# Kernel optimization log

Hardware: AMD Instinct MI355X
Metric: run time of the kernel (lower is better)

Reference implementation:

```python
import jax, jax.numpy as jnp
import numpy as np

B, N, NC, DIM, H, D, M, TOPK = 1, 2048, 2048, 1024, 16, 64, 16, 64


def _l2norm(t):
    # F.normalize(t, p=2, dim=-1)
    return t / jnp.clip(jnp.linalg.norm(t, axis=-1, keepdims=True), 1e-12)


def _attn_layer(x, ctx, q_mask, k_mask, Wq, Wk, Wv, th_pre, th_post,
                mem_k, mem_v, scale_p, hs, Wo):
    b, n, _ = x.shape
    h, m, d = mem_k.shape
    nc = ctx.shape[1]
    q = (x @ Wq).reshape(b, n, h, d).transpose(0, 2, 1, 3)      # b h i d
    k = (ctx @ Wk).reshape(b, nc, h, d).transpose(0, 2, 1, 3)   # b h j d
    v = (ctx @ Wv).reshape(b, nc, h, d).transpose(0, 2, 1, 3)
    # memory key/values prepended
    k = jnp.concatenate([jnp.broadcast_to(mem_k[None], (b, h, m, d)), k], axis=2)
    v = jnp.concatenate([jnp.broadcast_to(mem_v[None], (b, h, m, d)), v], axis=2)
    # input mask (q_mask x k_mask), padded True over mem slots
    im = q_mask[:, None, :, None] & k_mask[:, None, None, :]    # b 1 i j
    im = jnp.pad(im, ((0, 0), (0, 0), (0, 0), (m, 0)), constant_values=True)
    # qk_norm: cosine-sim attention with learned per-head scale
    q = _l2norm(q)
    k = _l2norm(k)
    scale = 1.0 / jnp.clip(jnp.exp(scale_p), 0.01)              # [h]
    dots = jnp.einsum('bhid,bhjd->bhij', q, k) * scale[None, :, None, None]
    dots = jnp.einsum('gh,bhij->bgij', th_pre, dots)            # pre-softmax talking heads (1x1 conv over heads)
    neg = -jnp.finfo(dots.dtype).max
    dots = jnp.where(im, dots, neg)
    # sparse topk: keep only the TOPK largest logits per query
    kth = jax.lax.top_k(dots, TOPK)[0][..., -1:]
    dots = jnp.where(dots < kth, neg, dots)
    attn = jax.nn.softmax(dots, axis=-1)
    attn = jnp.einsum('gh,bhij->bgij', th_post, attn)           # post-softmax talking heads
    out = jnp.einsum('bhij,bhjd->bhid', attn, v)
    out = out * hs[None, :, None, None]                          # head scale
    out = out.transpose(0, 2, 1, 3).reshape(b, n, h * d)
    return out @ Wo


def setup_inputs():
    key = jax.random.key(0)
    ks = jax.random.split(key, 18)
    s = 1.0 / np.sqrt(DIM)
    sh = 1.0 / np.sqrt(H)

    def w(i, shape, scale=1.0):
        return jax.random.normal(ks[i], shape, dtype=jnp.float32) * scale

    return {
        'x': w(0, (B, N, DIM)),
        'context': w(1, (2, B, NC, DIM)),
        'mask': jnp.ones((B, N), dtype=bool),
        'context_mask': jnp.ones((B, NC), dtype=bool),
        'Wq1': w(2, (DIM, H * D), s), 'Wk1': w(3, (DIM, H * D), s), 'Wv1': w(4, (DIM, H * D), s),
        'Wq2': w(5, (DIM, H * D), s), 'Wk2': w(6, (DIM, H * D), s), 'Wv2': w(7, (DIM, H * D), s),
        'th_pre1': w(8, (H, H), sh), 'th_post1': w(9, (H, H), sh),
        'th_pre2': w(10, (H, H), sh), 'th_post2': w(11, (H, H), sh),
        'mem_k1': w(12, (H, M, D)), 'mem_v1': w(13, (H, M, D)),
        'mem_k2': w(14, (H, M, D)), 'mem_v2': w(15, (H, M, D)),
        'scale1': jnp.full((H,), -3.0, jnp.float32),
        'scale2': jnp.full((H,), -3.0, jnp.float32),
        'head_scale1': jnp.ones((H,), jnp.float32),
        'head_scale2': jnp.ones((H,), jnp.float32),
        'Wo1': w(16, (H * D, DIM), s), 'Wo2': w(17, (H * D, DIM), s),
    }


def reference(x, context, mask, context_mask,
              Wq1, Wk1, Wv1, Wq2, Wk2, Wv2,
              th_pre1, th_post1, th_pre2, th_post2,
              mem_k1, mem_v1, mem_k2, mem_v2,
              scale1, scale2, head_scale1, head_scale2, Wo1, Wo2):
    x = _attn_layer(x, context[0], mask, context_mask, Wq1, Wk1, Wv1,
                    th_pre1, th_post1, mem_k1, mem_v1, scale1, head_scale1, Wo1)
    x = _attn_layer(x, context[1], mask, context_mask, Wq2, Wk2, Wv2,
                    th_pre2, th_post2, mem_k2, mem_v2, scale2, head_scale2, Wo2)
    return x
```

## Files before the change

### kernel.cpp

```cpp
#include <hip/hip_runtime.h>

#define DEVI __device__ __forceinline__

typedef unsigned short u16;
typedef __attribute__((ext_vector_type(8))) _Float16 f16x8;
typedef __attribute__((ext_vector_type(4))) float f32x4;

#define NQ   2048
#define DIMM 1024
#define HD   16
#define MM   16
#define JTOT 2064
#define JPK  2080
#define JPAD 2112
#define KTOP 64

DEVI u16 f2h(float x) {
    _Float16 h = (_Float16)x;
    u16 r; __builtin_memcpy(&r, &h, 2); return r;
}
DEVI void fsplit(float x, u16& hi, u16& lo) {
    _Float16 h = (_Float16)x;
    float r = x - (float)h;
    _Float16 l = (_Float16)r;
    __builtin_memcpy(&hi, &h, 2);
    __builtin_memcpy(&lo, &l, 2);
}

__global__ __launch_bounds__(256) void split1_kernel(
    const float* __restrict__ s, u16* __restrict__ hi, u16* __restrict__ lo, int n4)
{
    int gid = blockIdx.x * 256 + threadIdx.x;
    if (gid < n4) {
        float4 v = ((const float4*)s)[gid];
        ushort4 h, l;
        fsplit(v.x, h.x, l.x); fsplit(v.y, h.y, l.y);
        fsplit(v.z, h.z, l.z); fsplit(v.w, h.w, l.w);
        ((ushort4*)hi)[gid] = h;
        ((ushort4*)lo)[gid] = l;
    }
}

struct P8 { const float* w[8]; };

__global__ __launch_bounds__(256) void wtrans_kernel(P8 src, u16* WTh, u16* WTl) {
    __shared__ float T[64][65];
    const float* W = src.w[blockIdx.z];
    size_t off = (size_t)blockIdx.z * DIMM * DIMM;
    int n0 = blockIdx.x * 64, k0 = blockIdx.y * 64;
#pragma unroll
    for (int rep = 0; rep < 16; ++rep) {
        int idx = rep * 256 + threadIdx.x;
        int kk = idx >> 6, nn = idx & 63;
        T[kk][nn] = W[(size_t)(k0 + kk) * DIMM + n0 + nn];
    }
    __syncthreads();
#pragma unroll
    for (int rep = 0; rep < 16; ++rep) {
        int idx = rep * 256 + threadIdx.x;
        int nn = idx >> 6, kk = idx & 63;
        u16 h, l; fsplit(T[kk][nn], h, l);
        WTh[off + (size_t)(n0 + nn) * DIMM + k0 + kk] = h;
        WTl[off + (size_t)(n0 + nn) * DIMM + k0 + kk] = l;
    }
}

template<int OM>
__global__ __launch_bounds__(256) void gemm_nt(
    const u16* __restrict__ A, int lda, long sA,
    const u16* __restrict__ B, int ldb, long sB,
    void* __restrict__ Cv, int ldc, long sC, int K)
{
    __shared__ u16 As[64 * 40];
    __shared__ u16 Bs[64 * 40];
    const int tid = threadIdx.x;
    const int z = blockIdx.z;
    A += (size_t)z * sA; B += (size_t)z * sB;
    const int bm = blockIdx.x * 64, bn = blockIdx.y * 64;
    const int l = tid & 63, w = tid >> 6;
    const int wm = (w >> 1) * 32, wn = (w & 1) * 32;
    const int srow = tid >> 2, skcol = (tid & 3) * 8;
    const u16* Ag = A + (size_t)(bm + srow) * lda + skcol;
    const u16* Bg = B + (size_t)(bn + srow) * ldb + skcol;
    const int lr = l & 15, lk = (l >> 4) * 8;
    f32x4 acc[2][2] = {};
    for (int k0 = 0; k0 < K; k0 += 32) {
        uint4 av = *(const uint4*)(Ag + k0);
        uint4 bv = *(const uint4*)(Bg + k0);
        __syncthreads();
        *(uint4*)&As[srow * 40 + skcol] = av;
        *(uint4*)&Bs[srow * 40 + skcol] = bv;
        __syncthreads();
        f16x8 a0 = *(const f16x8*)&As[(wm + lr) * 40 + lk];
        f16x8 a1 = *(const f16x8*)&As[(wm + 16 + lr) * 40 + lk];
        f16x8 b0 = *(const f16x8*)&Bs[(wn + lr) * 40 + lk];
        f16x8 b1 = *(const f16x8*)&Bs[(wn + 16 + lr) * 40 + lk];
        acc[0][0] = __builtin_amdgcn_mfma_f32_16x16x32_f16(a0, b0, acc[0][0], 0, 0, 0);
        acc[0][1] = __builtin_amdgcn_mfma_f32_16x16x32_f16(a0, b1, acc[0][1], 0, 0, 0);
        acc[1][0] = __builtin_amdgcn_mfma_f32_16x16x32_f16(a1, b0, acc[1][0], 0, 0, 0);
        acc[1][1] = __builtin_amdgcn_mfma_f32_16x16x32_f16(a1, b1, acc[1][1], 0, 0, 0);
    }
    const int crow0 = bm + wm + (l >> 4) * 4;
    const int ccol0 = bn + wn + lr;
#pragma unroll
    for (int mi = 0; mi < 2; ++mi)
#pragma unroll
        for (int ni = 0; ni < 2; ++ni)
#pragma unroll
            for (int r = 0; r < 4; ++r) {
                int row = crow0 + mi * 16 + r;
                int col = ccol0 + ni * 16;
                if (OM == 0) {
                    float* C = (float*)Cv + (size_t)z * sC;
                    C[(size_t)row * ldc + col] = acc[mi][ni][r];
                } else {
                    u16* C = (u16*)Cv + (size_t)z * sC;
                    C[(size_t)row * ldc + col] = f2h(acc[mi][ni][r]);
                }
            }
}

__global__ __launch_bounds__(256) void gemm3_nt(
    const u16* __restrict__ Ah, const u16* __restrict__ Al, int lda,
    const u16* __restrict__ Bh, const u16* __restrict__ Bl, int ldb,
    float* __restrict__ C, int ldc, int K)
{
    __shared__ u16 Ash[64 * 40];
    __shared__ u16 Asl[64 * 40];
    __shared__ u16 Bsh[64 * 40];
    __shared__ u16 Bsl[64 * 40];
    const int tid = threadIdx.x;
    const int bm = blockIdx.x * 64, bn = blockIdx.y * 64;
    const int l = tid & 63, w = tid >> 6;
    const int wm = (w >> 1) * 32, wn = (w & 1) * 32;
    const int srow = tid >> 2, skcol = (tid & 3) * 8;
    const size_t aoff = (size_t)(bm + srow) * lda + skcol;
    const size_t boff = (size_t)(bn + srow) * ldb + skcol;
    const int lr = l & 15, lk = (l >> 4) * 8;
    f32x4 acc[2][2] = {};
    for (int k0 = 0; k0 < K; k0 += 32) {
        uint4 avh = *(const uint4*)(Ah + aoff + k0);
        uint4 avl = *(const uint4*)(Al + aoff + k0);
        uint4 bvh = *(const uint4*)(Bh + boff + k0);
        uint4 bvl = *(const uint4*)(Bl + boff + k0);
        __syncthreads();
        *(uint4*)&Ash[srow * 40 + skcol] = avh;
        *(uint4*)&Asl[srow * 40 + skcol] = avl;
        *(uint4*)&Bsh[srow * 40 + skcol] = bvh;
        *(uint4*)&Bsl[srow * 40 + skcol] = bvl;
        __syncthreads();
        f16x8 a0h = *(const f16x8*)&Ash[(wm + lr) * 40 + lk];
        f16x8 a1h = *(const f16x8*)&Ash[(wm + 16 + lr) * 40 + lk];
        f16x8 a0l = *(const f16x8*)&Asl[(wm + lr) * 40 + lk];
        f16x8 a1l = *(const f16x8*)&Asl[(wm + 16 + lr) * 40 + lk];
        f16x8 b0h = *(const f16x8*)&Bsh[(wn + lr) * 40 + lk];
        f16x8 b1h = *(const f16x8*)&Bsh[(wn + 16 + lr) * 40 + lk];
        f16x8 b0l = *(const f16x8*)&Bsl[(wn + lr) * 40 + lk];
        f16x8 b1l = *(const f16x8*)&Bsl[(wn + 16 + lr) * 40 + lk];
#define MF(acc_, a_, b_) acc_ = __builtin_amdgcn_mfma_f32_16x16x32_f16(a_, b_, acc_, 0, 0, 0)
        MF(acc[0][0], a0h, b0h); MF(acc[0][0], a0h, b0l); MF(acc[0][0], a0l, b0h);
        MF(acc[0][1], a0h, b1h); MF(acc[0][1], a0h, b1l); MF(acc[0][1], a0l, b1h);
        MF(acc[1][0], a1h, b0h); MF(acc[1][0], a1h, b0l); MF(acc[1][0], a1l, b0h);
        MF(acc[1][1], a1h, b1h); MF(acc[1][1], a1h, b1l); MF(acc[1][1], a1l, b1h);
#undef MF
    }
    const int crow0 = bm + wm + (l >> 4) * 4;
    const int ccol0 = bn + wn + lr;
#pragma unroll
    for (int mi = 0; mi < 2; ++mi)
#pragma unroll
        for (int ni = 0; ni < 2; ++ni)
#pragma unroll
            for (int r = 0; r < 4; ++r)
                C[(size_t)(crow0 + mi * 16 + r) * ldc + ccol0 + ni * 16] = acc[mi][ni][r];
}

__global__ __launch_bounds__(256) void normq_kernel(
    const float* __restrict__ Qf, const float* __restrict__ scp,
    u16* __restrict__ qnh, u16* __restrict__ qnl)
{
    int w = threadIdx.x >> 6, l = threadIdx.x & 63;
    int wid = blockIdx.x * 4 + w;
    int h = wid >> 11, i = wid & 2047;
    float x = Qf[(size_t)i * DIMM + h * 64 + l];
    float ss = x * x;
#pragma unroll
    for (int m = 32; m; m >>= 1) ss += __shfl_xor(ss, m);
    float inv = 1.0f / fmaxf(sqrtf(ss), 1e-12f);
    float sc = 1.0f / fmaxf(expf(scp[h]), 0.01f);
    u16 hh, ll; fsplit(x * inv * sc, hh, ll);
    size_t idx = ((size_t)h * NQ + i) * 64 + l;
    qnh[idx] = hh; qnl[idx] = ll;
}

__global__ __launch_bounds__(256) void buildkn_kernel(
    const float* __restrict__ Kf, const float* __restrict__ mem_k,
    u16* __restrict__ knh, u16* __restrict__ knl)
{
    int w = threadIdx.x >> 6, l = threadIdx.x & 63;
    int wid = blockIdx.x * 4 + w;
    int h = wid / JPK, j = wid - h * JPK;
    float x = (j < MM) ? mem_k[((size_t)h * MM + j) * 64 + l]
            : (j < JTOT) ? Kf[(size_t)(j - MM) * DIMM + h * 64 + l] : 0.0f;
    float ss = x * x;
#pragma unroll
    for (int m = 32; m; m >>= 1) ss += __shfl_xor(ss, m);
    float inv = 1.0f / fmaxf(sqrtf(ss), 1e-12f);
    u16 hh, ll; fsplit(x * inv, hh, ll);
    size_t idx = ((size_t)h * JPK + j) * 64 + l;
    knh[idx] = hh; knl[idx] = ll;
}

__global__ __launch_bounds__(256) void buildvvT_kernel(
    const float* __restrict__ Vf, const float* __restrict__ mem_v,
    const float* __restrict__ hsp, u16* __restrict__ vvT)
{
    __shared__ float T[64][65];
    int h = blockIdx.z, j0 = blockIdx.x * 64;
    float hs = hsp[h];
#pragma unroll
    for (int rep = 0; rep < 16; ++rep) {
        int idx = rep * 256 + threadIdx.x;
        int jl = idx >> 6, d = idx & 63;
        int j = j0 + jl;
        float x = (j < MM) ? mem_v[((size_t)h * MM + j) * 64 + d]
                : (j < JTOT) ? Vf[(size_t)(j - MM) * DIMM + h * 64 + d] : 0.0f;
        T[jl][d] = x * hs;
    }
    __syncthreads();
#pragma unroll
    for (int rep = 0; rep < 16; ++rep) {
        int idx = rep * 256 + threadIdx.x;
        int d = idx >> 6, jl = idx & 63;
        vvT[((size_t)h * 64 + d) * JPAD + j0 + jl] = f2h(T[jl][d]);
    }
}

__global__ __launch_bounds__(256) void dots_kernel(
    const u16* __restrict__ qnh, const u16* __restrict__ qnl,
    const u16* __restrict__ knh, const u16* __restrict__ knl,
    const float* __restrict__ th_pre, float* __restrict__ D,
    int q0, int NQC)
{
    __shared__ float red[4][8][256];
    const int tid = threadIdx.x, l = tid & 63, w = tid >> 6;
    const int it = blockIdx.x * 16;
    const int jt = blockIdx.y * 16;
    const int lr = l & 15, lk = (l >> 4) * 8;
    const int qrow = q0 + it + lr;
    const int jrow = jt + lr;
    f32x4 accg[16] = {};
#pragma unroll
    for (int hh = 0; hh < 4; ++hh) {
        const int h = w * 4 + hh;
        size_t qo = (((size_t)h * NQ + qrow) << 6) + lk;
        size_t ko = (((size_t)h * JPK + jrow) << 6) + lk;
        const f16x8* pah = (const f16x8*)(qnh + qo);
        const f16x8* pal = (const f16x8*)(qnl + qo);
        const f16x8* pbh = (const f16x8*)(knh + ko);
        const f16x8* pbl = (const f16x8*)(knl + ko);
        f16x8 a0h = pah[0], a1h = pah[4];
        f16x8 a0l = pal[0], a1l = pal[4];
        f16x8 b0h = pbh[0], b1h = pbh[4];
        f16x8 b0l = pbl[0], b1l = pbl[4];
        f32x4 ah = {};
        ah = __builtin_amdgcn_mfma_f32_16x16x32_f16(a0h, b0h, ah, 0, 0, 0);
        ah = __builtin_amdgcn_mfma_f32_16x16x32_f16(a1h, b1h, ah, 0, 0, 0);
        ah = __builtin_amdgcn_mfma_f32_16x16x32_f16(a0h, b0l, ah, 0, 0, 0);
        ah = __builtin_amdgcn_mfma_f32_16x16x32_f16(a1h, b1l, ah, 0, 0, 0);
        ah = __builtin_amdgcn_mfma_f32_16x16x32_f16(a0l, b0h, ah, 0, 0, 0);
        ah = __builtin_amdgcn_mfma_f32_16x16x32_f16(a1l, b1h, ah, 0, 0, 0);
#pragma unroll
        for (int g = 0; g < 16; ++g)
            accg[g] += th_pre[g * 16 + h] * ah;
    }
    const int orow = it + (l >> 4) * 4;
    const int col = jt + lr;
#pragma unroll
    for (int ph = 0; ph < 2; ++ph) {
        __syncthreads();
#pragma unroll
        for (int g = 0; g < 8; ++g)
            *(f32x4*)&red[w][g][l * 4] = accg[ph * 8 + g];
        __syncthreads();
#pragma unroll
        for (int gq = 0; gq < 2; ++gq) {
            const int gl = w * 2 + gq;
            f32x4 s = *(const f32x4*)&red[0][gl][l * 4];
            s += *(const f32x4*)&red[1][gl][l * 4];
            s += *(const f32x4*)&red[2][gl][l * 4];
            s += *(const f32x4*)&red[3][gl][l * 4];
            const int g = ph * 8 + gl;
#pragma unroll
            for (int r = 0; r < 4; ++r)
                D[((size_t)g * NQC + orow + r) * JPAD + col] = s[r];
        }
    }
}

__global__ __launch_bounds__(256) void rowstats_kernel(
    const float* __restrict__ D, float4* __restrict__ stats)
{
    const int w = threadIdx.x >> 6, l = threadIdx.x & 63;
    const int r = blockIdx.x * 4 + w;
    const float* Dr = D + (size_t)r * JPAD;
    float v[33]; unsigned ku[33];
#pragma unroll
    for (int s = 0; s < 33; ++s) {
        int j = s * 64 + l;
        float x = (j < JTOT) ? Dr[j] : -3.0e38f;
        v[s] = x;
        unsigned u = __float_as_uint(x);
        ku[s] = (j < JTOT) ? ((u & 0x80000000u) ? ~u : (u | 0x80000000u)) : 0u;
    }
    unsigned t = 0;
    for (int b = 31; b >= 0; --b) {
        unsigned tc = t | (1u << b);
        int c = 0;
#pragma unroll
        for (int s = 0; s < 33; ++s) c += (ku[s] >= tc);
#pragma unroll
        for (int m = 32; m; m >>= 1) c += __shfl_xor(c, m);
        if (c >= KTOP) t = tc;
    }
    float mx = v[0];
#pragma unroll
    for (int s = 1; s < 33; ++s) mx = fmaxf(mx, v[s]);
#pragma unroll
    for (int m = 32; m; m >>= 1) mx = fmaxf(mx, __shfl_xor(mx, m));
    float den = 0.0f;
#pragma unroll
    for (int s = 0; s < 33; ++s) den += (ku[s] >= t) ? __expf(v[s] - mx) : 0.0f;
#pragma unroll
    for (int m = 32; m; m >>= 1) den += __shfl_xor(den, m);
    if (l == 0) {
        float kth = (t & 0x80000000u) ? __uint_as_float(t ^ 0x80000000u)
                                      : __uint_as_float(~t);
        stats[r] = make_float4(kth, mx, 1.0f / den, 0.0f);
    }
}

__global__ __launch_bounds__(256) void probsmix_kernel(
    const float* __restrict__ D, const float4* __restrict__ stats,
    const float* __restrict__ th_post, u16* __restrict__ P, int NQC)
{
    int gid = blockIdx.x * 256 + threadIdx.x;
    int i = gid / 528;
    int jj = (gid - i * 528) * 4;
    f32x4 pm[16] = {};
    if (jj < JTOT) {
#pragma unroll
        for (int h = 0; h < 16; ++h) {
            float4 x = *(const float4*)(D + ((size_t)h * NQC + i) * JPAD + jj);
            float4 s = stats[h * NQC + i];
            f32x4 p;
            p[0] = (x.x >= s.x) ? __expf(x.x - s.y) * s.z : 0.0f;
            p[1] = (x.y >= s.x) ? __expf(x.y - s.y) * s.z : 0.0f;
            p[2] = (x.z >= s.x) ? __expf(x.z - s.y) * s.z : 0.0f;
            p[3] = (x.w >= s.x) ? __expf(x.w - s.y) * s.z : 0.0f;
#pragma unroll
            for (int g = 0; g < 16; ++g)
                pm[g] += th_post[g * 16 + h] * p;
        }
    }
#pragma unroll
    for (int g = 0; g < 16; ++g) {
        ushort4 o;
        o.x = f2h(pm[g][0]); o.y = f2h(pm[g][1]);
        o.z = f2h(pm[g][2]); o.w = f2h(pm[g][3]);
        *(ushort4*)(P + ((size_t)g * NQC + i) * JPAD + jj) = o;
    }
}

extern "C" void kernel_launch(void* const* d_in, const int* in_sizes, int n_in,
                              void* d_out, int out_size, void* d_ws, size_t ws_size,
                              hipStream_t stream)
{
    (void)in_sizes; (void)n_in; (void)out_size;
    const float* x      = (const float*)d_in[0];
    const float* ctx    = (const float*)d_in[1];
    const float* Wq1    = (const float*)d_in[4];
    const float* Wk1    = (const float*)d_in[5];
    const float* Wv1    = (const float*)d_in[6];
    const float* Wq2    = (const float*)d_in[7];
    const float* Wk2    = (const float*)d_in[8];
    const float* Wv2    = (const float*)d_in[9];
    const float* thpre1 = (const float*)d_in[10];
    const float* thpost1= (const float*)d_in[11];
    const float* thpre2 = (const float*)d_in[12];
    const float* thpost2= (const float*)d_in[13];
    const float* memk1  = (const float*)d_in[14];
    const float* memv1  = (const float*)d_in[15];
    const float* memk2  = (const float*)d_in[16];
    const float* memv2  = (const float*)d_in[17];
    const float* sc1    = (const float*)d_in[18];
    const float* sc2    = (const float*)d_in[19];
    const float* hs1    = (const float*)d_in[20];
    const float* hs2    = (const float*)d_in[21];
    const float* Wo1    = (const float*)d_in[22];
    const float* Wo2    = (const float*)d_in[23];

    char* p = (char*)d_ws;
    auto alloc = [&](size_t n) { char* r = p; p += (n + 255) & ~(size_t)255; return r; };
    u16*   xbh   = (u16*)alloc((size_t)NQ * DIMM * 2);
    u16*   xbl   = (u16*)alloc((size_t)NQ * DIMM * 2);
    u16*   cb0h  = (u16*)alloc((size_t)NQ * DIMM * 2);
    u16*   cb0l  = (u16*)alloc((size_t)NQ * DIMM * 2);
    u16*   cb1h  = (u16*)alloc((size_t)NQ * DIMM * 2);
    u16*   cb1l  = (u16*)alloc((size_t)NQ * DIMM * 2);
    u16*   WTh   = (u16*)alloc((size_t)8 * DIMM * DIMM * 2);
    u16*   WTl   = (u16*)alloc((size_t)8 * DIMM * DIMM * 2);
    float* Qf    = (float*)alloc((size_t)NQ * DIMM * 4);
    float* Kf    = (float*)alloc((size_t)NQ * DIMM * 4);
    float* Vf    = (float*)alloc((size_t)NQ * DIMM * 4);
    u16*   qnh   = (u16*)alloc((size_t)16 * NQ * 64 * 2);
    u16*   qnl   = (u16*)alloc((size_t)16 * NQ * 64 * 2);
    u16*   knh   = (u16*)alloc((size_t)16 * JPK * 64 * 2);
    u16*   knl   = (u16*)alloc((size_t)16 * JPK * 64 * 2);
    u16*   vvT   = (u16*)alloc((size_t)16 * 64 * JPAD * 2);
    u16*   attnA = (u16*)alloc((size_t)NQ * DIMM * 2);
    float4* stats = (float4*)alloc((size_t)16 * NQ * 16);
    size_t used = (size_t)(p - (char*)d_ws);

    int NQC = 32;
    for (int cand : {512, 256, 128, 64}) {
        if (used + (size_t)16 * cand * JPAD * 6 + 1024 <= ws_size) { NQC = cand; break; }
    }
    float* Dbuf = (float*)alloc((size_t)16 * NQC * JPAD * 4);
    u16*   Pbuf = (u16*)alloc((size_t)16 * NQC * JPAD * 2);

    const int N4 = (NQ * DIMM) / 4;
    split1_kernel<<<2048, 256, 0, stream>>>(x, xbh, xbl, N4);
    split1_kernel<<<2048, 256, 0, stream>>>(ctx, cb0h, cb0l, N4);
    split1_kernel<<<2048, 256, 0, stream>>>(ctx + (size_t)NQ * DIMM, cb1h, cb1l, N4);
    P8 w8{ { Wq1, Wk1, Wv1, Wo1, Wq2, Wk2, Wv2, Wo2 } };
    wtrans_kernel<<<dim3(16, 16, 8), 256, 0, stream>>>(w8, WTh, WTl);

    auto layer = [&](const u16* inh, const u16* inl,
                     const u16* ctxh, const u16* ctxl, int wbase,
                     const float* thpre, const float* thpost,
                     const float* memk, const float* memv,
                     const float* scp, const float* hsp, int li) {
        size_t o_q = (size_t)(wbase + 0) * DIMM * DIMM;
        size_t o_k = (size_t)(wbase + 1) * DIMM * DIMM;
        size_t o_v = (size_t)(wbase + 2) * DIMM * DIMM;
        size_t o_o = (size_t)(wbase + 3) * DIMM * DIMM;
        gemm3_nt<<<dim3(32, 16), 256, 0, stream>>>(inh, inl, DIMM, WTh + o_q, WTl + o_q, DIMM, Qf, DIMM, DIMM);
        gemm3_nt<<<dim3(32, 16), 256, 0, stream>>>(ctxh, ctxl, DIMM, WTh + o_k, WTl + o_k, DIMM, Kf, DIMM, DIMM);
        gemm_nt<0><<<dim3(32, 16, 1), 256, 0, stream>>>(ctxh, DIMM, 0, WTh + o_v, DIMM, 0, Vf, DIMM, 0, DIMM);
        normq_kernel<<<(16 * NQ) / 4, 256, 0, stream>>>(Qf, scp, qnh, qnl);
        buildkn_kernel<<<(16 * JPK) / 4, 256, 0, stream>>>(Kf, memk, knh, knl);
        buildvvT_kernel<<<dim3(33, 1, 16), 256, 0, stream>>>(Vf, memv, hsp, vvT);
        int nch = NQ / NQC;
        for (int c = 0; c < nch; ++c) {
            int q0 = c * NQC;
            dots_kernel<<<dim3(NQC / 16, JTOT / 16), 256, 0, stream>>>(qnh, qnl, knh, knl, thpre, Dbuf, q0, NQC);
            rowstats_kernel<<<(16 * NQC) / 4, 256, 0, stream>>>(Dbuf, stats);
            probsmix_kernel<<<(NQC * 528) / 256, 256, 0, stream>>>(Dbuf, stats, thpost, Pbuf, NQC);
            gemm_nt<1><<<dim3(NQC / 64, 1, 16), 256, 0, stream>>>(
                Pbuf, JPAD, (long)NQC * JPAD, vvT, JPAD, (long)64 * JPAD,
                attnA + (size_t)q0 * DIMM, DIMM, 64, JPAD);
        }
        if (li == 0) {
            gemm_nt<0><<<dim3(32, 16, 1), 256, 0, stream>>>(attnA, DIMM, 0, WTh + o_o, DIMM, 0, Qf, DIMM, 0, DIMM);
            split1_kernel<<<2048, 256, 0, stream>>>(Qf, xbh, xbl, N4);
        } else {
            gemm_nt<0><<<dim3(32, 16, 1), 256, 0, stream>>>(attnA, DIMM, 0, WTh + o_o, DIMM, 0, d_out, DIMM, 0, DIMM);
        }
    };

    layer(xbh, xbl, cb0h, cb0l, 0, thpre1, thpost1, memk1, memv1, sc1, hs1, 0);
    layer(xbh, xbl, cb1h, cb1l, 4, thpre2, thpost2, memk2, memv2, sc2, hs2, 1);
}
```

Baseline: 1.752 ms.

## Fuse top-k row stats and post-softmax head mixing into one MFMA kernel

Merges the row-statistics kernel (top-k threshold, max, denominator) and the probability/head-mix kernel into a single kernel with one block per query row. The block keeps per-head stats in shared memory and does the 16x16 post-softmax head mix with an f16 MFMA instead of scalar FMAs. This drops a launch, the stats buffer round trip and scalar mixing work. In exchange the grid shrinks to NQC blocks, each looping over 16 heads serially four per wave, which may cut parallelism. The mixing weights and probabilities are now rounded to f16 before the MFMA, which lowers precision.

Measured after the change: 2.284 ms. +30.3%, slower.

```diff
diff --git a/kernel.cpp b/kernel.cpp
--- a/kernel.cpp
+++ b/kernel.cpp
@@ -298,77 +298,86 @@
     }
 }
 
-__global__ __launch_bounds__(256) void rowstats_kernel(
-    const float* __restrict__ D, float4* __restrict__ stats)
-{
-    const int w = threadIdx.x >> 6, l = threadIdx.x & 63;
-    const int r = blockIdx.x * 4 + w;
-    const float* Dr = D + (size_t)r * JPAD;
-    float v[33]; unsigned ku[33];
-#pragma unroll
-    for (int s = 0; s < 33; ++s) {
-        int j = s * 64 + l;
-        float x = (j < JTOT) ? Dr[j] : -3.0e38f;
-        v[s] = x;
-        unsigned u = __float_as_uint(x);
-        ku[s] = (j < JTOT) ? ((u & 0x80000000u) ? ~u : (u | 0x80000000u)) : 0u;
-    }
-    unsigned t = 0;
-    for (int b = 31; b >= 0; --b) {
-        unsigned tc = t | (1u << b);
-        int c = 0;
-#pragma unroll
-        for (int s = 0; s < 33; ++s) c += (ku[s] >= tc);
-#pragma unroll
-        for (int m = 32; m; m >>= 1) c += __shfl_xor(c, m);
-        if (c >= KTOP) t = tc;
-    }
-    float mx = v[0];
-#pragma unroll
-    for (int s = 1; s < 33; ++s) mx = fmaxf(mx, v[s]);
-#pragma unroll
-    for (int m = 32; m; m >>= 1) mx = fmaxf(mx, __shfl_xor(mx, m));
-    float den = 0.0f;
-#pragma unroll
-    for (int s = 0; s < 33; ++s) den += (ku[s] >= t) ? __expf(v[s] - mx) : 0.0f;
-#pragma unroll
-    for (int m = 32; m; m >>= 1) den += __shfl_xor(den, m);
-    if (l == 0) {
-        float kth = (t & 0x80000000u) ? __uint_as_float(t ^ 0x80000000u)
-                                      : __uint_as_float(~t);
-        stats[r] = make_float4(kth, mx, 1.0f / den, 0.0f);
-    }
-}
-
-__global__ __launch_bounds__(256) void probsmix_kernel(
-    const float* __restrict__ D, const float4* __restrict__ stats,
-    const float* __restrict__ th_post, u16* __restrict__ P, int NQC)
-{
-    int gid = blockIdx.x * 256 + threadIdx.x;
-    int i = gid / 528;
-    int jj = (gid - i * 528) * 4;
-    f32x4 pm[16] = {};
-    if (jj < JTOT) {
-#pragma unroll
-        for (int h = 0; h < 16; ++h) {
-            float4 x = *(const float4*)(D + ((size_t)h * NQC + i) * JPAD + jj);
-            float4 s = stats[h * NQC + i];
-            f32x4 p;
-            p[0] = (x.x >= s.x) ? __expf(x.x - s.y) * s.z : 0.0f;
-            p[1] = (x.y >= s.x) ? __expf(x.y - s.y) * s.z : 0.0f;
-            p[2] = (x.z >= s.x) ? __expf(x.z - s.y) * s.z : 0.0f;
-            p[3] = (x.w >= s.x) ? __expf(x.w - s.y) * s.z : 0.0f;
-#pragma unroll
-            for (int g = 0; g < 16; ++g)
-                pm[g] += th_post[g * 16 + h] * p;
-        }
-    }
-#pragma unroll
-    for (int g = 0; g < 16; ++g) {
-        ushort4 o;
-        o.x = f2h(pm[g][0]); o.y = f2h(pm[g][1]);
-        o.z = f2h(pm[g][2]); o.w = f2h(pm[g][3]);
-        *(ushort4*)(P + ((size_t)g * NQC + i) * JPAD + jj) = o;
+__global__ __launch_bounds__(256) void smfused_kernel(
+    const float* __restrict__ D, const float* __restrict__ th_post,
+    u16* __restrict__ P, int NQC)
+{
+    __shared__ float s_kth[16], s_mx[16], s_inv[16];
+    const int tid = threadIdx.x, l = tid & 63, w = tid >> 6;
+    const int i = blockIdx.x;
+    const size_t plane = (size_t)NQC * JPAD;
+    for (int hh = 0; hh < 4; ++hh) {
+        const int h = w * 4 + hh;
+        const float* Dr = D + (size_t)h * plane + (size_t)i * JPAD;
+        float v[33]; unsigned ku[33];
+#pragma unroll
+        for (int s = 0; s < 33; ++s) {
+            int j = s * 64 + l;
+            float x = (j < JTOT) ? Dr[j] : -3.0e38f;
+            v[s] = x;
+            unsigned u = __float_as_uint(x);
+            ku[s] = (j < JTOT) ? ((u & 0x80000000u) ? ~u : (u | 0x80000000u)) : 0u;
+        }
+        unsigned t = 0;
+        for (int b = 31; b >= 0; --b) {
+            unsigned tc = t | (1u << b);
+            int c = 0;
+#pragma unroll
+            for (int s = 0; s < 33; ++s) c += (ku[s] >= tc);
+#pragma unroll
+            for (int m = 32; m; m >>= 1) c += __shfl_xor(c, m);
+            if (c >= KTOP) t = tc;
+        }
+        float mx = v[0];
+#pragma unroll
+        for (int s = 1; s < 33; ++s) mx = fmaxf(mx, v[s]);
+#pragma unroll
+        for (int m = 32; m; m >>= 1) mx = fmaxf(mx, __shfl_xor(mx, m));
+        float den = 0.0f;
+#pragma unroll
+        for (int s = 0; s < 33; ++s) den += (ku[s] >= t) ? __expf(v[s] - mx) : 0.0f;
+#pragma unroll
+        for (int m = 32; m; m >>= 1) den += __shfl_xor(den, m);
+        if (l == 0) {
+            float kth = (t & 0x80000000u) ? __uint_as_float(t ^ 0x80000000u)
+                                          : __uint_as_float(~t);
+            s_kth[h] = kth; s_mx[h] = mx; s_inv[h] = 1.0f / den;
+        }
+    }
+    __syncthreads();
+    const int g = l & 15, hg = l >> 4;
+    const int hb = (hg & 1) * 8;
+    f16x8 afr;
+#pragma unroll
+    for (int idx = 0; idx < 8; ++idx) {
+        int k = hg * 8 + idx;
+        float av = (k < 16) ? th_post[g * 16 + k] : 0.0f;
+        afr[idx] = (_Float16)av;
+    }
+    float kthv[8], mxv[8], invv[8];
+#pragma unroll
+    for (int idx = 0; idx < 8; ++idx) {
+        kthv[idx] = s_kth[hb + idx];
+        mxv[idx]  = s_mx[hb + idx];
+        invv[idx] = s_inv[hb + idx];
+    }
+    const float* Dbase = D + (size_t)i * JPAD;
+    for (int t = w; t < 129; t += 4) {
+        const int j = t * 16 + (l & 15);
+        f16x8 bfr;
+#pragma unroll
+        for (int idx = 0; idx < 8; ++idx) {
+            float d = Dbase[(size_t)(hb + idx) * plane + j];
+            float e = (d >= kthv[idx]) ? __expf(d - mxv[idx]) * invv[idx] : 0.0f;
+            bfr[idx] = (_Float16)e;
+        }
+        f32x4 c = {};
+        c = __builtin_amdgcn_mfma_f32_16x16x32_f16(afr, bfr, c, 0, 0, 0);
+#pragma unroll
+        for (int r = 0; r < 4; ++r) {
+            const int gg = hg * 4 + r;
+            P[(size_t)gg * plane + (size_t)i * JPAD + j] = f2h(c[r]);
+        }
     }
 }
 
@@ -419,7 +428,6 @@
     u16*   knl   = (u16*)alloc((size_t)16 * JPK * 64 * 2);
     u16*   vvT   = (u16*)alloc((size_t)16 * 64 * JPAD * 2);
     u16*   attnA = (u16*)alloc((size_t)NQ * DIMM * 2);
-    float4* stats = (float4*)alloc((size_t)16 * NQ * 16);
     size_t used = (size_t)(p - (char*)d_ws);
 
     int NQC = 32;
@@ -455,8 +463,7 @@
         for (int c = 0; c < nch; ++c) {
             int q0 = c * NQC;
             dots_kernel<<<dim3(NQC / 16, JTOT / 16), 256, 0, stream>>>(qnh, qnl, knh, knl, thpre, Dbuf, q0, NQC);
-            rowstats_kernel<<<(16 * NQC) / 4, 256, 0, stream>>>(Dbuf, stats);
-            probsmix_kernel<<<(NQC * 528) / 256, 256, 0, stream>>>(Dbuf, stats, thpost, Pbuf, NQC);
+            smfused_kernel<<<NQC, 256, 0, stream>>>(Dbuf, thpost, Pbuf, NQC);
             gemm_nt<1><<<dim3(NQC / 64, 1, 16), 256, 0, stream>>>(
                 Pbuf, JPAD, (long)NQC * JPAD, vvT, JPAD, (long)64 * JPAD,
                 attnA + (size_t)q0 * DIMM, DIMM, 64, JPAD);
```
